# Optimization experiments

Measured on AMD Instinct MI355X. Metric: run time of the kernel, lower is better.

Reference implementation:

```python
import jax, jax.numpy as jnp
import numpy as np

E, T, D_H, D_I, R = 8, 4096, 2048, 5632, 128


def setup_inputs() -> dict:
    key = jax.random.key(0)
    ks = jax.random.split(key, 12)
    s = 0.02
    return {
        "x": jax.random.normal(ks[0], (T, D_H), dtype=jnp.float32),
        "expert_idx": jax.random.randint(ks[1], (T,), 0, E),
        # gate: hidden -> intermediate
        "gate_A": jax.random.normal(ks[2], (E, R, D_H), dtype=jnp.float32) * s,
        "gate_C": jax.random.normal(ks[3], (R, R), dtype=jnp.float32) * s,
        "gate_B": jax.random.normal(ks[4], (E, D_I, R), dtype=jnp.float32) * s,
        # up: hidden -> intermediate
        "up_A": jax.random.normal(ks[5], (E, R, D_H), dtype=jnp.float32) * s,
        "up_C": jax.random.normal(ks[6], (R, R), dtype=jnp.float32) * s,
        "up_B": jax.random.normal(ks[7], (E, D_I, R), dtype=jnp.float32) * s,
        # down: intermediate -> hidden, with per-expert bias
        "down_A": jax.random.normal(ks[8], (E, R, D_I), dtype=jnp.float32) * s,
        "down_C": jax.random.normal(ks[9], (R, R), dtype=jnp.float32) * s,
        "down_B": jax.random.normal(ks[10], (E, D_H, R), dtype=jnp.float32) * s,
        "down_bias": jax.random.normal(ks[11], (E, D_H), dtype=jnp.float32) * s,
    }


def _shared_core(x, A, C, B, onehot_et):
    # x: [t, d_in]; A: [e, r, d_in]; C: [r, r]; B: [e, d_out, r]; onehot_et: [e, t]
    # per-token expert weight W_e = B_e @ C @ A_e; mask early so zeros propagate
    h = jnp.einsum('td,erd->etr', x, A) * onehot_et[:, :, None]  # [e, t, r]
    h = jnp.einsum('etr,sr->ets', h, C)                           # [e, t, r]
    return jnp.einsum('ets,eds->td', h, B)                        # [t, d_out]


def reference(x, expert_idx, gate_A, gate_C, gate_B, up_A, up_C, up_B,
              down_A, down_C, down_B, down_bias):
    onehot = jax.nn.one_hot(expert_idx, E, dtype=x.dtype).T  # [E, T]
    g = jax.nn.silu(_shared_core(x, gate_A, gate_C, gate_B, onehot))  # [T, D_I]
    u = _shared_core(x, up_A, up_C, up_B, onehot)                     # [T, D_I]
    down = _shared_core(g * u, down_A, down_C, down_B, onehot)        # [T, D_H]
    return down + down_bias[expert_idx]
```

## Files before the change

### kernel.cpp

```cpp
#include <hip/hip_runtime.h>
#include <hip/hip_bf16.h>

#define E_  8
#define T_  4096
#define DH_ 2048
#define DI_ 5632
#define R_  128
#define TILE_ 32
#define NT_ 136
#define TPMAX_ (NT_*TILE_)

typedef short bf16x8 __attribute__((ext_vector_type(8)));
typedef short bf16x4 __attribute__((ext_vector_type(4)));
typedef float f32x4 __attribute__((ext_vector_type(4)));

#define MFMA(a, b, c) __builtin_amdgcn_mfma_f32_16x16x32_bf16((a), (b), (c), 0, 0, 0)

__device__ __forceinline__ unsigned short f2bf(float f) {
  union { float f; unsigned u; } v; v.f = f;
  return (unsigned short)((v.u + 0x7fffu + ((v.u >> 16) & 1u)) >> 16);
}

__device__ __forceinline__ bf16x8 cvt8(float4 a, float4 b) {
  bf16x8 o;
  o[0] = (short)f2bf(a.x); o[1] = (short)f2bf(a.y);
  o[2] = (short)f2bf(a.z); o[3] = (short)f2bf(a.w);
  o[4] = (short)f2bf(b.x); o[5] = (short)f2bf(b.y);
  o[6] = (short)f2bf(b.z); o[7] = (short)f2bf(b.w);
  return o;
}

__device__ __forceinline__ int tile_expert(int s0, const int* off) {
  int e = 0;
#pragma unroll
  for (int q = 1; q < E_; q++) if (s0 >= off[q]) e = q;
  return e;
}

__global__ void k_count(const int* __restrict__ idx, int* __restrict__ cnt) {
  int t = blockIdx.x * 256 + threadIdx.x;
  if (t < T_) atomicAdd(&cnt[idx[t]], 1);
}

__global__ void k_offsets(const int* __restrict__ cnt, int* __restrict__ off,
                          int* __restrict__ cur) {
  if (threadIdx.x == 0) {
    int a = 0;
    for (int e = 0; e < E_; e++) {
      off[e] = a; cur[e] = a;
      a += ((cnt[e] + TILE_ - 1) / TILE_) * TILE_;
    }
    off[E_] = a;
  }
}

__global__ void k_scatter(const int* __restrict__ idx, int* __restrict__ cur,
                          int* __restrict__ tok) {
  int t = blockIdx.x * 256 + threadIdx.x;
  if (t < T_) {
    int p = atomicAdd(&cur[idx[t]], 1);
    tok[p] = t;
  }
}

__global__ __launch_bounds__(256) void k_cvt(
    const float* __restrict__ gA, const float* __restrict__ uA,
    const float* __restrict__ gB, const float* __restrict__ uB,
    const float* __restrict__ dA, const float* __restrict__ dB,
    const float* __restrict__ gC, const float* __restrict__ uC,
    const float* __restrict__ dC,
    short* __restrict__ gAb, short* __restrict__ uAb,
    short* __restrict__ gBb, short* __restrict__ uBb,
    short* __restrict__ dAb, short* __restrict__ dBb,
    short* __restrict__ gCb, short* __restrict__ uCb,
    short* __restrict__ dCb)
{
  long i = (long)(blockIdx.x * 256 + threadIdx.x) * 4;
  const float* s; short* d;
  if      (i <  4194304) { if (i < 2097152) { s = gA; d = gAb; } else { s = uA; d = uAb; i -= 2097152; } }
  else if (i <  9961472) { s = gB; d = gBb; i -= 4194304; }
  else if (i < 15728640) { s = uB; d = uBb; i -= 9961472; }
  else if (i < 21495808) { s = dA; d = dAb; i -= 15728640; }
  else if (i < 23592960) { s = dB; d = dBb; i -= 21495808; }
  else if (i < 23609344) { s = gC; d = gCb; i -= 23592960; }
  else if (i < 23625728) { s = uC; d = uCb; i -= 23609344; }
  else if (i < 23642112) { s = dC; d = dCb; i -= 23625728; }
  else return;
  float4 v = *(const float4*)(s + i);
  bf16x4 o;
  o[0] = (short)f2bf(v.x); o[1] = (short)f2bf(v.y);
  o[2] = (short)f2bf(v.z); o[3] = (short)f2bf(v.w);
  *(bf16x4*)(d + i) = o;
}

__global__ __launch_bounds__(256) void k_gather(
    const float* __restrict__ x, const int* __restrict__ tok,
    short* __restrict__ Xb)
{
  const int p = blockIdx.x;
  const int t = tok[p];
  const int c = threadIdx.x * 8;
  bf16x8 o;
  if (t >= 0) {
    float4 v0 = *(const float4*)(x + (size_t)t * DH_ + c);
    float4 v1 = *(const float4*)(x + (size_t)t * DH_ + c + 4);
    o = cvt8(v0, v1);
  } else {
    o = (bf16x8){0, 0, 0, 0, 0, 0, 0, 0};
  }
  *(bf16x8*)(Xb + (size_t)p * DH_ + c) = o;
}

__global__ __launch_bounds__(256) void k_stage1(
    const short* __restrict__ Xb,
    const short* __restrict__ gAb, const short* __restrict__ uAb,
    const int* __restrict__ off, float* __restrict__ Hp)
{
  const int s0 = blockIdx.x * TILE_;
  if (s0 >= off[E_]) return;
  const int e = tile_expert(s0, off);
  const int y = blockIdx.y, kc = blockIdx.z;
  const short* A = (y ? uAb : gAb) + (size_t)e * R_ * DH_ + kc * 512;

  const int tid = threadIdx.x;
  const int lane = tid & 63, wv = tid >> 6;
  const int col = lane & 15, quad = lane >> 4;

  const short* x0 = Xb + (size_t)(s0 + col) * DH_ + kc * 512 + quad * 8;
  const short* x1 = x0 + (size_t)16 * DH_;
  const short* Ab0 = A + (size_t)(wv * 32 + col) * DH_ + quad * 8;
  const short* Ab1 = Ab0 + (size_t)16 * DH_;

  f32x4 acc[2][2] = {};
#pragma unroll 4
  for (int k0 = 0; k0 < 512; k0 += 32) {
    bf16x8 a0 = *(const bf16x8*)(x0 + k0);
    bf16x8 a1 = *(const bf16x8*)(x1 + k0);
    bf16x8 b0 = *(const bf16x8*)(Ab0 + k0);
    bf16x8 b1 = *(const bf16x8*)(Ab1 + k0);
    acc[0][0] = MFMA(a0, b0, acc[0][0]);
    acc[0][1] = MFMA(a0, b1, acc[0][1]);
    acc[1][0] = MFMA(a1, b0, acc[1][0]);
    acc[1][1] = MFMA(a1, b1, acc[1][1]);
  }
  float* O = Hp + (size_t)(y * 4 + kc) * TPMAX_ * R_;
#pragma unroll
  for (int m = 0; m < 2; m++)
#pragma unroll
    for (int nl = 0; nl < 2; nl++)
#pragma unroll
      for (int r = 0; r < 4; r++)
        O[(size_t)(s0 + m * 16 + quad * 4 + r) * R_ + (wv * 2 + nl) * 16 + col] =
            acc[m][nl][r];
}

__global__ __launch_bounds__(256) void k_stage1b(
    const float* __restrict__ Hp,
    const short* __restrict__ gCb, const short* __restrict__ uCb,
    const int* __restrict__ off,
    short* __restrict__ Hgb, short* __restrict__ Hub)
{
  const int s0 = blockIdx.x * TILE_;
  if (s0 >= off[E_]) return;
  const int y = blockIdx.y;
  const short* C = y ? uCb : gCb;
  short* H = y ? Hub : Hgb;

  __shared__ short h1s[32][136];
  const int tid = threadIdx.x;
  {
    const int lg = tid >> 3, lq = (tid & 7) * 16;
    const float* base = Hp + ((size_t)y * 4 * TPMAX_ + s0 + lg) * R_ + lq;
    float s[16] = {};
#pragma unroll
    for (int kc = 0; kc < 4; kc++) {
      const float* p = base + (size_t)kc * TPMAX_ * R_;
#pragma unroll
      for (int q = 0; q < 4; q++) {
        float4 v = *(const float4*)(p + q * 4);
        s[q * 4 + 0] += v.x; s[q * 4 + 1] += v.y;
        s[q * 4 + 2] += v.z; s[q * 4 + 3] += v.w;
      }
    }
#pragma unroll
    for (int j = 0; j < 16; j++) h1s[lg][lq + j] = (short)f2bf(s[j]);
  }
  __syncthreads();

  const int lane = tid & 63, wv = tid >> 6;
  const int col = lane & 15, quad = lane >> 4;
  f32x4 acc2[2][2] = {};
#pragma unroll
  for (int kk = 0; kk < 4; kk++) {
    bf16x8 a0 = *(const bf16x8*)&h1s[col][kk * 32 + quad * 8];
    bf16x8 a1 = *(const bf16x8*)&h1s[16 + col][kk * 32 + quad * 8];
#pragma unroll
    for (int nl = 0; nl < 2; nl++) {
      bf16x8 b = *(const bf16x8*)(C + (size_t)((wv * 2 + nl) * 16 + col) * R_ +
                                  kk * 32 + quad * 8);
      acc2[0][nl] = MFMA(a0, b, acc2[0][nl]);
      acc2[1][nl] = MFMA(a1, b, acc2[1][nl]);
    }
  }
#pragma unroll
  for (int m = 0; m < 2; m++)
#pragma unroll
    for (int nl = 0; nl < 2; nl++)
#pragma unroll
      for (int r = 0; r < 4; r++)
        H[(size_t)(s0 + m * 16 + quad * 4 + r) * R_ + (wv * 2 + nl) * 16 + col] =
            (short)f2bf(acc2[m][nl][r]);
}

__global__ __launch_bounds__(256) void k_stage2(
    const short* __restrict__ Hgb, const short* __restrict__ Hub,
    const short* __restrict__ gBb, const short* __restrict__ uBb,
    const short* __restrict__ dAb,
    const int* __restrict__ off, float* __restrict__ Hd1)
{
  const int s0 = blockIdx.x * TILE_;
  if (s0 >= off[E_]) return;
  const int e = tile_expert(s0, off);
  const int i0 = blockIdx.y * 512;
  const short* Bg = gBb + (size_t)e * DI_ * R_;
  const short* Bu = uBb + (size_t)e * DI_ * R_;
  const short* Ad = dAb + (size_t)e * R_ * DI_;

  __shared__ short ZT[32][136];

  const int tid = threadIdx.x;
  const int lane = tid & 63, wv = tid >> 6;
  const int col = lane & 15, quad = lane >> 4;

  bf16x8 hg[2][4], hu[2][4];
#pragma unroll
  for (int m = 0; m < 2; m++)
#pragma unroll
    for (int kk = 0; kk < 4; kk++) {
      size_t o = (size_t)(s0 + m * 16 + col) * R_ + kk * 32 + quad * 8;
      hg[m][kk] = *(const bf16x8*)(Hgb + o);
      hu[m][kk] = *(const bf16x8*)(Hub + o);
    }

  f32x4 dacc[2][2] = {};

  for (int sc = 0; sc < 4; sc++) {
    const int ib = i0 + sc * 128;
    f32x4 gacc[2][2] = {}, uacc[2][2] = {};
#pragma unroll
    for (int kk = 0; kk < 4; kk++) {
#pragma unroll
      for (int nl = 0; nl < 2; nl++) {
        size_t bo = (size_t)(ib + (wv * 2 + nl) * 16 + col) * R_ + kk * 32 + quad * 8;
        bf16x8 bg = *(const bf16x8*)(Bg + bo);
        bf16x8 bu = *(const bf16x8*)(Bu + bo);
#pragma unroll
        for (int m = 0; m < 2; m++) {
          gacc[m][nl] = MFMA(hg[m][kk], bg, gacc[m][nl]);
          uacc[m][nl] = MFMA(hu[m][kk], bu, uacc[m][nl]);
        }
      }
    }
    __syncthreads();
#pragma unroll
    for (int m = 0; m < 2; m++)
#pragma unroll
      for (int nl = 0; nl < 2; nl++)
#pragma unroll
        for (int r = 0; r < 4; r++) {
          float g = gacc[m][nl][r];
          float z = (g / (1.0f + __expf(-g))) * uacc[m][nl][r];
          ZT[m * 16 + quad * 4 + r][(wv * 2 + nl) * 16 + col] = (short)f2bf(z);
        }
    __syncthreads();
#pragma unroll
    for (int kk2 = 0; kk2 < 4; kk2++) {
      bf16x8 za0 = *(const bf16x8*)&ZT[col][kk2 * 32 + quad * 8];
      bf16x8 za1 = *(const bf16x8*)&ZT[16 + col][kk2 * 32 + quad * 8];
#pragma unroll
      for (int nl = 0; nl < 2; nl++) {
        bf16x8 ba = *(const bf16x8*)(Ad + (size_t)((wv * 2 + nl) * 16 + col) * DI_ +
                                     ib + kk2 * 32 + quad * 8);
        dacc[0][nl] = MFMA(za0, ba, dacc[0][nl]);
        dacc[1][nl] = MFMA(za1, ba, dacc[1][nl]);
      }
    }
  }
#pragma unroll
  for (int m = 0; m < 2; m++)
#pragma unroll
    for (int nl = 0; nl < 2; nl++)
#pragma unroll
      for (int r = 0; r < 4; r++)
        atomicAdd(&Hd1[(size_t)(s0 + m * 16 + quad * 4 + r) * R_ + (wv * 2 + nl) * 16 + col],
                  dacc[m][nl][r]);
}

__global__ __launch_bounds__(256) void k_stage3(
    const float* __restrict__ Hd1, const short* __restrict__ dCb,
    const short* __restrict__ dBb, const float* __restrict__ dbias,
    const int* __restrict__ off, const int* __restrict__ tok,
    float* __restrict__ out)
{
  const int s0 = blockIdx.x * TILE_;
  if (s0 >= off[E_]) return;
  const int e = tile_expert(s0, off);
  const int d0 = blockIdx.y * 128;

  __shared__ short h2s[32][136];
  const int tid = threadIdx.x;
  const int lane = tid & 63, wv = tid >> 6;
  const int col = lane & 15, quad = lane >> 4;

  f32x4 acc2[2][2] = {};
#pragma unroll
  for (int kk = 0; kk < 4; kk++) {
    bf16x8 a[2];
#pragma unroll
    for (int m = 0; m < 2; m++) {
      const float* hp = Hd1 + (size_t)(s0 + m * 16 + col) * R_ + kk * 32 + quad * 8;
      float4 v0 = *(const float4*)hp;
      float4 v1 = *(const float4*)(hp + 4);
      a[m] = cvt8(v0, v1);
    }
#pragma unroll
    for (int nl = 0; nl < 2; nl++) {
      bf16x8 b = *(const bf16x8*)(dCb + (size_t)((wv * 2 + nl) * 16 + col) * R_ +
                                  kk * 32 + quad * 8);
      acc2[0][nl] = MFMA(a[0], b, acc2[0][nl]);
      acc2[1][nl] = MFMA(a[1], b, acc2[1][nl]);
    }
  }
#pragma unroll
  for (int m = 0; m < 2; m++)
#pragma unroll
    for (int nl = 0; nl < 2; nl++)
#pragma unroll
      for (int r = 0; r < 4; r++)
        h2s[m * 16 + quad * 4 + r][(wv * 2 + nl) * 16 + col] = (short)f2bf(acc2[m][nl][r]);
  __syncthreads();

  f32x4 acc3[2][2] = {};
#pragma unroll
  for (int kk = 0; kk < 4; kk++) {
    bf16x8 a0 = *(const bf16x8*)&h2s[col][kk * 32 + quad * 8];
    bf16x8 a1 = *(const bf16x8*)&h2s[16 + col][kk * 32 + quad * 8];
#pragma unroll
    for (int nl = 0; nl < 2; nl++) {
      bf16x8 b = *(const bf16x8*)(dBb + (size_t)e * DH_ * R_ +
                                  (size_t)(d0 + (wv * 2 + nl) * 16 + col) * R_ +
                                  kk * 32 + quad * 8);
      acc3[0][nl] = MFMA(a0, b, acc3[0][nl]);
      acc3[1][nl] = MFMA(a1, b, acc3[1][nl]);
    }
  }
  float bias[2];
#pragma unroll
  for (int nl = 0; nl < 2; nl++)
    bias[nl] = dbias[(size_t)e * DH_ + d0 + (wv * 2 + nl) * 16 + col];
#pragma unroll
  for (int m = 0; m < 2; m++)
#pragma unroll
    for (int r = 0; r < 4; r++) {
      int t = tok[s0 + m * 16 + quad * 4 + r];
      if (t < 0) continue;
#pragma unroll
      for (int nl = 0; nl < 2; nl++) {
        int d = d0 + (wv * 2 + nl) * 16 + col;
        out[(size_t)t * DH_ + d] = acc3[m][nl][r] + bias[nl];
      }
    }
}

extern "C" void kernel_launch(void* const* d_in, const int* in_sizes, int n_in,
                              void* d_out, int out_size, void* d_ws, size_t ws_size,
                              hipStream_t stream)
{
  (void)in_sizes; (void)n_in; (void)out_size; (void)ws_size;
  const float* x     = (const float*)d_in[0];
  const int*   idx   = (const int*)d_in[1];
  const float* gA    = (const float*)d_in[2];
  const float* gC    = (const float*)d_in[3];
  const float* gBw   = (const float*)d_in[4];
  const float* uA    = (const float*)d_in[5];
  const float* uC    = (const float*)d_in[6];
  const float* uBw   = (const float*)d_in[7];
  const float* dA    = (const float*)d_in[8];
  const float* dC    = (const float*)d_in[9];
  const float* dBw   = (const float*)d_in[10];
  const float* dbias = (const float*)d_in[11];
  float* out = (float*)d_out;

  char* ws = (char*)d_ws;
  int* cnt = (int*)ws;
  int* cur = cnt + 8;
  int* off = cnt + 16;
  int* tok = (int*)(ws + 512);
  float* Hd1 = (float*)(ws + 32768);
  float* Hp  = (float*)(ws + 2260992);
  short* Xb  = (short*)(ws + 20086784);
  short* Hgb = (short*)(ws + 37912576);
  short* Hub = (short*)(ws + 39026688);
  short* gAb = (short*)(ws + 40140800);
  short* uAb = (short*)(ws + 44335104);
  short* gBb = (short*)(ws + 48529408);
  short* uBb = (short*)(ws + 60063744);
  short* dAb = (short*)(ws + 71598080);
  short* dBb = (short*)(ws + 83132416);
  short* gCb = (short*)(ws + 87326720);
  short* uCb = (short*)(ws + 87359488);
  short* dCb = (short*)(ws + 87392256);

  hipMemsetAsync(d_ws, 0, 128, stream);
  hipMemsetAsync(tok, 0xFF, TPMAX_ * sizeof(int), stream);
  hipMemsetAsync(Hd1, 0, (size_t)TPMAX_ * R_ * sizeof(float), stream);

  k_cvt    <<<dim3(23088), 256, 0, stream>>>(gA, uA, gBw, uBw, dA, dBw, gC, uC, dC,
                                             gAb, uAb, gBb, uBb, dAb, dBb, gCb, uCb, dCb);
  k_count  <<<dim3(T_ / 256), 256, 0, stream>>>(idx, cnt);
  k_offsets<<<1, 64, 0, stream>>>(cnt, off, cur);
  k_scatter<<<dim3(T_ / 256), 256, 0, stream>>>(idx, cur, tok);
  k_gather <<<dim3(TPMAX_), 256, 0, stream>>>(x, tok, Xb);
  k_stage1 <<<dim3(NT_, 2, 4), 256, 0, stream>>>(Xb, gAb, uAb, off, Hp);
  k_stage1b<<<dim3(NT_, 2), 256, 0, stream>>>(Hp, gCb, uCb, off, Hgb, Hub);
  k_stage2 <<<dim3(NT_, 11), 256, 0, stream>>>(Hgb, Hub, gBb, uBb, dAb, off, Hd1);
  k_stage3 <<<dim3(NT_, 16), 256, 0, stream>>>(Hd1, dCb, dBb, dbias, off, tok, out);
}
```

Baseline: 388.8 us.

## Double token tile to 64 rows and fuse routing kernels into one block

Grows the per-block token tile from 32 to 64 rows in every stage, so each weight fragment loaded from global memory feeds four MFMA row-blocks instead of two. Stage2 now stages the gate/up hidden rows in shared memory rather than holding them in registers. The three routing kernels (count, offsets, scatter) are merged into a single 1024-thread block that uses shared-memory atomics, which removes two launches and one memset. The larger tile adds more padding per expert and fewer blocks, and raises register and LDS use, which could reduce occupancy.

Measured after the change: 334.7 us. 1.16x faster.

```diff
diff --git a/kernel.cpp b/kernel.cpp
--- a/kernel.cpp
+++ b/kernel.cpp
@@ -6,8 +6,8 @@
 #define DH_ 2048
 #define DI_ 5632
 #define R_  128
-#define TILE_ 32
-#define NT_ 136
+#define TILE_ 64
+#define NT_ 72
 #define TPMAX_ (NT_*TILE_)
 
 typedef short bf16x8 __attribute__((ext_vector_type(8)));
@@ -37,27 +37,26 @@
   return e;
 }
 
-__global__ void k_count(const int* __restrict__ idx, int* __restrict__ cnt) {
-  int t = blockIdx.x * 256 + threadIdx.x;
-  if (t < T_) atomicAdd(&cnt[idx[t]], 1);
-}
-
-__global__ void k_offsets(const int* __restrict__ cnt, int* __restrict__ off,
-                          int* __restrict__ cur) {
-  if (threadIdx.x == 0) {
+__global__ __launch_bounds__(1024) void k_route(
+    const int* __restrict__ idx, int* __restrict__ off, int* __restrict__ tok)
+{
+  __shared__ int cnt[E_], cur[E_], offs[E_ + 1];
+  const int tid = threadIdx.x;
+  if (tid < E_) cnt[tid] = 0;
+  __syncthreads();
+  for (int t = tid; t < T_; t += 1024) atomicAdd(&cnt[idx[t]], 1);
+  __syncthreads();
+  if (tid == 0) {
     int a = 0;
     for (int e = 0; e < E_; e++) {
-      off[e] = a; cur[e] = a;
+      offs[e] = a; cur[e] = a;
       a += ((cnt[e] + TILE_ - 1) / TILE_) * TILE_;
     }
-    off[E_] = a;
-  }
-}
-
-__global__ void k_scatter(const int* __restrict__ idx, int* __restrict__ cur,
-                          int* __restrict__ tok) {
-  int t = blockIdx.x * 256 + threadIdx.x;
-  if (t < T_) {
+    offs[E_] = a;
+  }
+  __syncthreads();
+  if (tid <= E_) off[tid] = offs[tid];
+  for (int t = tid; t < T_; t += 1024) {
     int p = atomicAdd(&cur[idx[t]], 1);
     tok[p] = t;
   }
@@ -126,26 +125,24 @@
   const int lane = tid & 63, wv = tid >> 6;
   const int col = lane & 15, quad = lane >> 4;
 
-  const short* x0 = Xb + (size_t)(s0 + col) * DH_ + kc * 512 + quad * 8;
-  const short* x1 = x0 + (size_t)16 * DH_;
-  const short* Ab0 = A + (size_t)(wv * 32 + col) * DH_ + quad * 8;
-  const short* Ab1 = Ab0 + (size_t)16 * DH_;
-
-  f32x4 acc[2][2] = {};
+  const short* xb = Xb + (size_t)(s0 + col) * DH_ + kc * 512 + quad * 8;
+  const short* ab = A + (size_t)(wv * 32 + col) * DH_ + quad * 8;
+
+  f32x4 acc[4][2] = {};
 #pragma unroll 4
   for (int k0 = 0; k0 < 512; k0 += 32) {
-    bf16x8 a0 = *(const bf16x8*)(x0 + k0);
-    bf16x8 a1 = *(const bf16x8*)(x1 + k0);
-    bf16x8 b0 = *(const bf16x8*)(Ab0 + k0);
-    bf16x8 b1 = *(const bf16x8*)(Ab1 + k0);
-    acc[0][0] = MFMA(a0, b0, acc[0][0]);
-    acc[0][1] = MFMA(a0, b1, acc[0][1]);
-    acc[1][0] = MFMA(a1, b0, acc[1][0]);
-    acc[1][1] = MFMA(a1, b1, acc[1][1]);
+    bf16x8 b0 = *(const bf16x8*)(ab + k0);
+    bf16x8 b1 = *(const bf16x8*)(ab + (size_t)16 * DH_ + k0);
+#pragma unroll
+    for (int m = 0; m < 4; m++) {
+      bf16x8 a = *(const bf16x8*)(xb + (size_t)m * 16 * DH_ + k0);
+      acc[m][0] = MFMA(a, b0, acc[m][0]);
+      acc[m][1] = MFMA(a, b1, acc[m][1]);
+    }
   }
   float* O = Hp + (size_t)(y * 4 + kc) * TPMAX_ * R_;
 #pragma unroll
-  for (int m = 0; m < 2; m++)
+  for (int m = 0; m < 4; m++)
 #pragma unroll
     for (int nl = 0; nl < 2; nl++)
 #pragma unroll
@@ -166,44 +163,46 @@
   const short* C = y ? uCb : gCb;
   short* H = y ? Hub : Hgb;
 
-  __shared__ short h1s[32][136];
+  __shared__ short h1s[64][136];
   const int tid = threadIdx.x;
   {
-    const int lg = tid >> 3, lq = (tid & 7) * 16;
+    const int lg = tid >> 2, lq = (tid & 3) * 32;
     const float* base = Hp + ((size_t)y * 4 * TPMAX_ + s0 + lg) * R_ + lq;
-    float s[16] = {};
+    float s[32] = {};
 #pragma unroll
     for (int kc = 0; kc < 4; kc++) {
       const float* p = base + (size_t)kc * TPMAX_ * R_;
 #pragma unroll
-      for (int q = 0; q < 4; q++) {
+      for (int q = 0; q < 8; q++) {
         float4 v = *(const float4*)(p + q * 4);
         s[q * 4 + 0] += v.x; s[q * 4 + 1] += v.y;
         s[q * 4 + 2] += v.z; s[q * 4 + 3] += v.w;
       }
     }
 #pragma unroll
-    for (int j = 0; j < 16; j++) h1s[lg][lq + j] = (short)f2bf(s[j]);
+    for (int j = 0; j < 32; j++) h1s[lg][lq + j] = (short)f2bf(s[j]);
   }
   __syncthreads();
 
   const int lane = tid & 63, wv = tid >> 6;
   const int col = lane & 15, quad = lane >> 4;
-  f32x4 acc2[2][2] = {};
+  f32x4 acc2[4][2] = {};
 #pragma unroll
   for (int kk = 0; kk < 4; kk++) {
-    bf16x8 a0 = *(const bf16x8*)&h1s[col][kk * 32 + quad * 8];
-    bf16x8 a1 = *(const bf16x8*)&h1s[16 + col][kk * 32 + quad * 8];
-#pragma unroll
-    for (int nl = 0; nl < 2; nl++) {
-      bf16x8 b = *(const bf16x8*)(C + (size_t)((wv * 2 + nl) * 16 + col) * R_ +
-                                  kk * 32 + quad * 8);
-      acc2[0][nl] = MFMA(a0, b, acc2[0][nl]);
-      acc2[1][nl] = MFMA(a1, b, acc2[1][nl]);
-    }
-  }
-#pragma unroll
-  for (int m = 0; m < 2; m++)
+    bf16x8 b[2];
+#pragma unroll
+    for (int nl = 0; nl < 2; nl++)
+      b[nl] = *(const bf16x8*)(C + (size_t)((wv * 2 + nl) * 16 + col) * R_ +
+                               kk * 32 + quad * 8);
+#pragma unroll
+    for (int m = 0; m < 4; m++) {
+      bf16x8 a = *(const bf16x8*)&h1s[m * 16 + col][kk * 32 + quad * 8];
+      acc2[m][0] = MFMA(a, b[0], acc2[m][0]);
+      acc2[m][1] = MFMA(a, b[1], acc2[m][1]);
+    }
+  }
+#pragma unroll
+  for (int m = 0; m < 4; m++)
 #pragma unroll
     for (int nl = 0; nl < 2; nl++)
 #pragma unroll
@@ -226,44 +225,54 @@
   const short* Bu = uBb + (size_t)e * DI_ * R_;
   const short* Ad = dAb + (size_t)e * R_ * DI_;
 
-  __shared__ short ZT[32][136];
+  __shared__ short hgs[64][136];
+  __shared__ short hus[64][136];
+  __shared__ short ZT[64][136];
 
   const int tid = threadIdx.x;
   const int lane = tid & 63, wv = tid >> 6;
   const int col = lane & 15, quad = lane >> 4;
 
-  bf16x8 hg[2][4], hu[2][4];
-#pragma unroll
-  for (int m = 0; m < 2; m++)
-#pragma unroll
-    for (int kk = 0; kk < 4; kk++) {
-      size_t o = (size_t)(s0 + m * 16 + col) * R_ + kk * 32 + quad * 8;
-      hg[m][kk] = *(const bf16x8*)(Hgb + o);
-      hu[m][kk] = *(const bf16x8*)(Hub + o);
-    }
-
-  f32x4 dacc[2][2] = {};
+  {
+    const int row = tid >> 2, seg = (tid & 3) * 32;
+    const short* pg = Hgb + (size_t)(s0 + row) * R_ + seg;
+    const short* pu = Hub + (size_t)(s0 + row) * R_ + seg;
+#pragma unroll
+    for (int q = 0; q < 4; q++) {
+      *(bf16x8*)&hgs[row][seg + q * 8] = *(const bf16x8*)(pg + q * 8);
+      *(bf16x8*)&hus[row][seg + q * 8] = *(const bf16x8*)(pu + q * 8);
+    }
+  }
+  __syncthreads();
+
+  f32x4 dacc[4][2] = {};
 
   for (int sc = 0; sc < 4; sc++) {
     const int ib = i0 + sc * 128;
-    f32x4 gacc[2][2] = {}, uacc[2][2] = {};
+    f32x4 gacc[4][2] = {}, uacc[4][2] = {};
 #pragma unroll
     for (int kk = 0; kk < 4; kk++) {
+      bf16x8 bg[2], bu[2];
 #pragma unroll
       for (int nl = 0; nl < 2; nl++) {
         size_t bo = (size_t)(ib + (wv * 2 + nl) * 16 + col) * R_ + kk * 32 + quad * 8;
-        bf16x8 bg = *(const bf16x8*)(Bg + bo);
-        bf16x8 bu = *(const bf16x8*)(Bu + bo);
-#pragma unroll
-        for (int m = 0; m < 2; m++) {
-          gacc[m][nl] = MFMA(hg[m][kk], bg, gacc[m][nl]);
-          uacc[m][nl] = MFMA(hu[m][kk], bu, uacc[m][nl]);
+        bg[nl] = *(const bf16x8*)(Bg + bo);
+        bu[nl] = *(const bf16x8*)(Bu + bo);
+      }
+#pragma unroll
+      for (int m = 0; m < 4; m++) {
+        bf16x8 ag = *(const bf16x8*)&hgs[m * 16 + col][kk * 32 + quad * 8];
+        bf16x8 au = *(const bf16x8*)&hus[m * 16 + col][kk * 32 + quad * 8];
+#pragma unroll
+        for (int nl = 0; nl < 2; nl++) {
+          gacc[m][nl] = MFMA(ag, bg[nl], gacc[m][nl]);
+          uacc[m][nl] = MFMA(au, bu[nl], uacc[m][nl]);
         }
       }
     }
     __syncthreads();
 #pragma unroll
-    for (int m = 0; m < 2; m++)
+    for (int m = 0; m < 4; m++)
 #pragma unroll
       for (int nl = 0; nl < 2; nl++)
 #pragma unroll
@@ -275,19 +284,21 @@
     __syncthreads();
 #pragma unroll
     for (int kk2 = 0; kk2 < 4; kk2++) {
-      bf16x8 za0 = *(const bf16x8*)&ZT[col][kk2 * 32 + quad * 8];
-      bf16x8 za1 = *(const bf16x8*)&ZT[16 + col][kk2 * 32 + quad * 8];
-#pragma unroll
-      for (int nl = 0; nl < 2; nl++) {
-        bf16x8 ba = *(const bf16x8*)(Ad + (size_t)((wv * 2 + nl) * 16 + col) * DI_ +
-                                     ib + kk2 * 32 + quad * 8);
-        dacc[0][nl] = MFMA(za0, ba, dacc[0][nl]);
-        dacc[1][nl] = MFMA(za1, ba, dacc[1][nl]);
+      bf16x8 ba[2];
+#pragma unroll
+      for (int nl = 0; nl < 2; nl++)
+        ba[nl] = *(const bf16x8*)(Ad + (size_t)((wv * 2 + nl) * 16 + col) * DI_ +
+                                  ib + kk2 * 32 + quad * 8);
+#pragma unroll
+      for (int m = 0; m < 4; m++) {
+        bf16x8 za = *(const bf16x8*)&ZT[m * 16 + col][kk2 * 32 + quad * 8];
+        dacc[m][0] = MFMA(za, ba[0], dacc[m][0]);
+        dacc[m][1] = MFMA(za, ba[1], dacc[m][1]);
       }
     }
   }
 #pragma unroll
-  for (int m = 0; m < 2; m++)
+  for (int m = 0; m < 4; m++)
 #pragma unroll
     for (int nl = 0; nl < 2; nl++)
 #pragma unroll
@@ -307,32 +318,31 @@
   const int e = tile_expert(s0, off);
   const int d0 = blockIdx.y * 128;
 
-  __shared__ short h2s[32][136];
+  __shared__ short h2s[64][136];
   const int tid = threadIdx.x;
   const int lane = tid & 63, wv = tid >> 6;
   const int col = lane & 15, quad = lane >> 4;
 
-  f32x4 acc2[2][2] = {};
+  f32x4 acc2[4][2] = {};
 #pragma unroll
   for (int kk = 0; kk < 4; kk++) {
-    bf16x8 a[2];
-#pragma unroll
-    for (int m = 0; m < 2; m++) {
+    bf16x8 b[2];
+#pragma unroll
+    for (int nl = 0; nl < 2; nl++)
+      b[nl] = *(const bf16x8*)(dCb + (size_t)((wv * 2 + nl) * 16 + col) * R_ +
+                               kk * 32 + quad * 8);
+#pragma unroll
+    for (int m = 0; m < 4; m++) {
       const float* hp = Hd1 + (size_t)(s0 + m * 16 + col) * R_ + kk * 32 + quad * 8;
       float4 v0 = *(const float4*)hp;
       float4 v1 = *(const float4*)(hp + 4);
-      a[m] = cvt8(v0, v1);
-    }
-#pragma unroll
-    for (int nl = 0; nl < 2; nl++) {
-      bf16x8 b = *(const bf16x8*)(dCb + (size_t)((wv * 2 + nl) * 16 + col) * R_ +
-                                  kk * 32 + quad * 8);
-      acc2[0][nl] = MFMA(a[0], b, acc2[0][nl]);
-      acc2[1][nl] = MFMA(a[1], b, acc2[1][nl]);
-    }
-  }
-#pragma unroll
-  for (int m = 0; m < 2; m++)
+      bf16x8 a = cvt8(v0, v1);
+      acc2[m][0] = MFMA(a, b[0], acc2[m][0]);
+      acc2[m][1] = MFMA(a, b[1], acc2[m][1]);
+    }
+  }
+#pragma unroll
+  for (int m = 0; m < 4; m++)
 #pragma unroll
     for (int nl = 0; nl < 2; nl++)
 #pragma unroll
@@ -340,18 +350,20 @@
         h2s[m * 16 + quad * 4 + r][(wv * 2 + nl) * 16 + col] = (short)f2bf(acc2[m][nl][r]);
   __syncthreads();
 
-  f32x4 acc3[2][2] = {};
+  f32x4 acc3[4][2] = {};
 #pragma unroll
   for (int kk = 0; kk < 4; kk++) {
-    bf16x8 a0 = *(const bf16x8*)&h2s[col][kk * 32 + quad * 8];
-    bf16x8 a1 = *(const bf16x8*)&h2s[16 + col][kk * 32 + quad * 8];
-#pragma unroll
-    for (int nl = 0; nl < 2; nl++) {
-      bf16x8 b = *(const bf16x8*)(dBb + (size_t)e * DH_ * R_ +
-                                  (size_t)(d0 + (wv * 2 + nl) * 16 + col) * R_ +
-                                  kk * 32 + quad * 8);
-      acc3[0][nl] = MFMA(a0, b, acc3[0][nl]);
-      acc3[1][nl] = MFMA(a1, b, acc3[1][nl]);
+    bf16x8 b[2];
+#pragma unroll
+    for (int nl = 0; nl < 2; nl++)
+      b[nl] = *(const bf16x8*)(dBb + (size_t)e * DH_ * R_ +
+                               (size_t)(d0 + (wv * 2 + nl) * 16 + col) * R_ +
+                               kk * 32 + quad * 8);
+#pragma unroll
+    for (int m = 0; m < 4; m++) {
+      bf16x8 a = *(const bf16x8*)&h2s[m * 16 + col][kk * 32 + quad * 8];
+      acc3[m][0] = MFMA(a, b[0], acc3[m][0]);
+      acc3[m][1] = MFMA(a, b[1], acc3[m][1]);
     }
   }
   float bias[2];
@@ -359,7 +371,7 @@
   for (int nl = 0; nl < 2; nl++)
     bias[nl] = dbias[(size_t)e * DH_ + d0 + (wv * 2 + nl) * 16 + col];
 #pragma unroll
-  for (int m = 0; m < 2; m++)
+  for (int m = 0; m < 4; m++)
 #pragma unroll
     for (int r = 0; r < 4; r++) {
       int t = tok[s0 + m * 16 + quad * 4 + r];
@@ -392,34 +404,29 @@
   float* out = (float*)d_out;
 
   char* ws = (char*)d_ws;
-  int* cnt = (int*)ws;
-  int* cur = cnt + 8;
-  int* off = cnt + 16;
+  int* off = (int*)ws;
   int* tok = (int*)(ws + 512);
   float* Hd1 = (float*)(ws + 32768);
-  float* Hp  = (float*)(ws + 2260992);
-  short* Xb  = (short*)(ws + 20086784);
-  short* Hgb = (short*)(ws + 37912576);
-  short* Hub = (short*)(ws + 39026688);
-  short* gAb = (short*)(ws + 40140800);
-  short* uAb = (short*)(ws + 44335104);
-  short* gBb = (short*)(ws + 48529408);
-  short* uBb = (short*)(ws + 60063744);
-  short* dAb = (short*)(ws + 71598080);
-  short* dBb = (short*)(ws + 83132416);
-  short* gCb = (short*)(ws + 87326720);
-  short* uCb = (short*)(ws + 87359488);
-  short* dCb = (short*)(ws + 87392256);
-
-  hipMemsetAsync(d_ws, 0, 128, stream);
+  float* Hp  = (float*)(ws + 2392064);
+  short* Xb  = (short*)(ws + 21266432);
+  short* Hgb = (short*)(ws + 40140800);
+  short* Hub = (short*)(ws + 41320448);
+  short* gAb = (short*)(ws + 42500096);
+  short* uAb = (short*)(ws + 46694400);
+  short* gBb = (short*)(ws + 50888704);
+  short* uBb = (short*)(ws + 62423040);
+  short* dAb = (short*)(ws + 73957376);
+  short* dBb = (short*)(ws + 85491712);
+  short* gCb = (short*)(ws + 89686016);
+  short* uCb = (short*)(ws + 89718784);
+  short* dCb = (short*)(ws + 89751552);
+
   hipMemsetAsync(tok, 0xFF, TPMAX_ * sizeof(int), stream);
   hipMemsetAsync(Hd1, 0, (size_t)TPMAX_ * R_ * sizeof(float), stream);
 
   k_cvt    <<<dim3(23088), 256, 0, stream>>>(gA, uA, gBw, uBw, dA, dBw, gC, uC, dC,
                                              gAb, uAb, gBb, uBb, dAb, dBb, gCb, uCb, dCb);
-  k_count  <<<dim3(T_ / 256), 256, 0, stream>>>(idx, cnt);
-  k_offsets<<<1, 64, 0, stream>>>(cnt, off, cur);
-  k_scatter<<<dim3(T_ / 256), 256, 0, stream>>>(idx, cur, tok);
+  k_route  <<<1, 1024, 0, stream>>>(idx, off, tok);
   k_gather <<<dim3(TPMAX_), 256, 0, stream>>>(x, tok, Xb);
   k_stage1 <<<dim3(NT_, 2, 4), 256, 0, stream>>>(Xb, gAb, uAb, off, Hp);
   k_stage1b<<<dim3(NT_, 2), 256, 0, stream>>>(Hp, gCb, uCb, off, Hgb, Hub);
```
